# Kernel tuning notes

Hardware: AMD Instinct MI355X
Metric: run time of the kernel (lower is better)

## Reference

```python
import jax, jax.numpy as jnp
import numpy as np
import math

B, S, H, NH, WIN = 2, 2048, 1024, 16, 1024
HD = H // NH


def _ln(x, g, b, eps=1e-5):
    mu = jnp.mean(x, axis=-1, keepdims=True)
    var = jnp.var(x, axis=-1, keepdims=True)
    return (x - mu) * jax.lax.rsqrt(var + eps) * g + b


def setup_inputs() -> dict:
    key = jax.random.key(0)
    ks = jax.random.split(key, 16)
    w = lambda k, shp: jax.random.normal(k, shp, dtype=jnp.float32) * 0.02
    d = {
        "hidden_states": jax.random.normal(ks[0], (B, S, H), dtype=jnp.float32),
        "window_pos_bias": jax.random.normal(ks[1], (1, NH, 2 * WIN + 1, 2 * WIN + 1), dtype=jnp.float32) * 0.02,
        # position_encoding: Linear(1->H) + LayerNorm(H)
        "pe_w": w(ks[2], (1, H)), "pe_b": jnp.zeros((H,), jnp.float32),
        "pe_g": jnp.ones((H,), jnp.float32), "pe_beta": jnp.zeros((H,), jnp.float32),
        # pre-attention LayerNorm
        "norm_g": jnp.ones((H,), jnp.float32), "norm_b": jnp.zeros((H,), jnp.float32),
        # QKV projections (stored as [in, out])
        "Wq": w(ks[3], (H, H)), "bq": jnp.zeros((H,), jnp.float32),
        "Wk": w(ks[4], (H, H)), "bk": jnp.zeros((H,), jnp.float32),
        "Wv": w(ks[5], (H, H)), "bv": jnp.zeros((H,), jnp.float32),
        # out_proj: Linear(H,2H)+LN+ReLU, Linear(2H,2H)+LN+ReLU, Linear(2H,2H)+LN+ReLU, Linear(2H,H)
        "W1": w(ks[6], (H, 2 * H)), "b1": jnp.zeros((2 * H,), jnp.float32),
        "g1": jnp.ones((2 * H,), jnp.float32), "be1": jnp.zeros((2 * H,), jnp.float32),
        "W2": w(ks[7], (2 * H, 2 * H)), "b2": jnp.zeros((2 * H,), jnp.float32),
        "g2": jnp.ones((2 * H,), jnp.float32), "be2": jnp.zeros((2 * H,), jnp.float32),
        "W3": w(ks[8], (2 * H, 2 * H)), "b3": jnp.zeros((2 * H,), jnp.float32),
        "g3": jnp.ones((2 * H,), jnp.float32), "be3": jnp.zeros((2 * H,), jnp.float32),
        "W4": w(ks[9], (2 * H, H)), "b4": jnp.zeros((H,), jnp.float32),
    }
    return d


def reference(hidden_states, window_pos_bias, pe_w, pe_b, pe_g, pe_beta,
              norm_g, norm_b, Wq, bq, Wk, bk, Wv, bv,
              W1, b1, g1, be1, W2, b2, g2, be2, W3, b3, g3, be3, W4, b4):
    b, s, h = hidden_states.shape
    nh = window_pos_bias.shape[1]
    hd = h // nh
    # relative positions in [-1, 1): (i - s//2) / (s//2 + 1e-6)
    mid = s // 2
    pos = ((jnp.arange(s, dtype=jnp.float32) - mid) / (mid + 1e-6))[:, None]  # [s,1]
    pe = _ln(pos @ pe_w + pe_b, pe_g, pe_beta)  # [s,h]  (dropout = identity in eval)
    x = _ln(hidden_states + pe[None], norm_g, norm_b)
    q = (x @ Wq + bq).reshape(b, s, nh, hd)
    k = (x @ Wk + bk).reshape(b, s, nh, hd)
    v = (x @ Wv + bv).reshape(b, s, nh, hd)
    scores = jnp.einsum('bqhd,bkhd->bhqk', q, k) / math.sqrt(hd)
    if s <= window_pos_bias.shape[-1]:
        scores = scores + window_pos_bias[:, :, :s, :s]
    attn = jax.nn.softmax(scores, axis=-1)
    ctx = jnp.einsum('bhqk,bkhd->bqhd', attn, v).reshape(b, s, h)
    y = jax.nn.relu(_ln(ctx @ W1 + b1, g1, be1))
    y = jax.nn.relu(_ln(y @ W2 + b2, g2, be2))
    y = jax.nn.relu(_ln(y @ W3 + b3, g3, be3))
    out = y @ W4 + b4
    return out
```

## Files before the change

### kernel.cpp

```cpp
#include <hip/hip_runtime.h>
#include <hip/hip_bf16.h>
#include <math.h>

typedef unsigned short u16;
typedef unsigned int u32;
typedef __bf16 v8bf __attribute__((ext_vector_type(8)));
typedef float v4f __attribute__((ext_vector_type(4)));

constexpr int BATCH = 2;
constexpr int SEQ = 2048;
constexpr int HID = 1024;
constexpr int NHEAD = 16;
constexpr int HDIM = 64;
constexpr int MROWS = BATCH * SEQ;
constexpr int BIAS_LD = 2 * 1024 + 1;
constexpr size_t BIAS_HSTRIDE = (size_t)BIAS_LD * BIAS_LD;

__device__ __forceinline__ u16 f2bf(float f) {
    u32 u = __builtin_bit_cast(u32, f);
    u32 r = u + 0x7fffu + ((u >> 16) & 1u);
    return (u16)(r >> 16);
}

__device__ __forceinline__ int swoff8(int row, int chunk)  { return (row * 8  + (chunk ^ (row & 7)))  << 4; }
__device__ __forceinline__ int swoff16(int row, int chunk) { return (row * 16 + (chunk ^ (row & 15))) << 4; }

__device__ __forceinline__ float2 blockreduce2(float a, float b) {
    #pragma unroll
    for (int m = 1; m < 64; m <<= 1) {
        a += __shfl_xor(a, m, 64);
        b += __shfl_xor(b, m, 64);
    }
    __shared__ float la[4], lb[4];
    int w = threadIdx.x >> 6;
    if ((threadIdx.x & 63) == 0) { la[w] = a; lb[w] = b; }
    __syncthreads();
    a = la[0] + la[1] + la[2] + la[3];
    b = lb[0] + lb[1] + lb[2] + lb[3];
    __syncthreads();
    return make_float2(a, b);
}

__global__ __launch_bounds__(256) void k_wt(const float* __restrict__ W, u16* __restrict__ Wt, int K, int N) {
    __shared__ float t[32][33];
    int n0 = blockIdx.x * 32, k0 = blockIdx.y * 32;
    int tx = threadIdx.x & 31, ty = threadIdx.x >> 5;
    #pragma unroll
    for (int i = 0; i < 32; i += 8) t[ty + i][tx] = W[(size_t)(k0 + ty + i) * N + n0 + tx];
    __syncthreads();
    #pragma unroll
    for (int i = 0; i < 32; i += 8) Wt[(size_t)(n0 + ty + i) * K + k0 + tx] = f2bf(t[tx][ty + i]);
}

__global__ __launch_bounds__(256) void k_prenorm(const float* __restrict__ hidden,
        const float* __restrict__ pe_w, const float* __restrict__ pe_b,
        const float* __restrict__ pe_g, const float* __restrict__ pe_beta,
        const float* __restrict__ ng, const float* __restrict__ nb, u16* __restrict__ xbf) {
    int row = blockIdx.x;
    int s = row & (SEQ - 1);
    float pos = ((float)s - 1024.0f) * (1.0f / 1024.0f);
    int t = threadIdx.x;
    float v[4];
    float s1 = 0.f, s2 = 0.f;
    #pragma unroll
    for (int i = 0; i < 4; i++) {
        int hh = i * 256 + t;
        float x = pos * pe_w[hh] + pe_b[hh];
        v[i] = x; s1 += x; s2 += x * x;
    }
    float2 red = blockreduce2(s1, s2);
    float mean = red.x * (1.f / HID);
    float var  = red.y * (1.f / HID) - mean * mean;
    float rstd = rsqrtf(var + 1e-5f);
    s1 = 0.f; s2 = 0.f;
    #pragma unroll
    for (int i = 0; i < 4; i++) {
        int hh = i * 256 + t;
        float pe = (v[i] - mean) * rstd * pe_g[hh] + pe_beta[hh];
        float x = hidden[(size_t)row * HID + hh] + pe;
        v[i] = x; s1 += x; s2 += x * x;
    }
    red = blockreduce2(s1, s2);
    mean = red.x * (1.f / HID);
    var  = red.y * (1.f / HID) - mean * mean;
    rstd = rsqrtf(var + 1e-5f);
    #pragma unroll
    for (int i = 0; i < 4; i++) {
        int hh = i * 256 + t;
        xbf[(size_t)row * HID + hh] = f2bf((v[i] - mean) * rstd * ng[hh] + nb[hh]);
    }
}

__global__ __launch_bounds__(256) void k_ln_relu(const float* __restrict__ Z,
        const float* __restrict__ g, const float* __restrict__ be, u16* __restrict__ Y, int N) {
    int row = blockIdx.x, t = threadIdx.x;
    float v[8];
    float s1 = 0.f, s2 = 0.f;
    int c = N >> 8;
    #pragma unroll
    for (int i = 0; i < 8; i++) {
        if (i < c) {
            int hh = i * 256 + t;
            float x = Z[(size_t)row * N + hh];
            v[i] = x; s1 += x; s2 += x * x;
        }
    }
    float2 red = blockreduce2(s1, s2);
    float inv = 1.0f / (float)N;
    float mean = red.x * inv;
    float var  = red.y * inv - mean * mean;
    float rstd = rsqrtf(var + 1e-5f);
    #pragma unroll
    for (int i = 0; i < 8; i++) {
        if (i < c) {
            int hh = i * 256 + t;
            float y = (v[i] - mean) * rstd * g[hh] + be[hh];
            Y[(size_t)row * N + hh] = f2bf(fmaxf(y, 0.f));
        }
    }
}

__global__ __launch_bounds__(256) void k_vtrans(const u16* __restrict__ V, u16* __restrict__ Vt) {
    __shared__ u16 t[64][68];
    int s0 = blockIdx.x * 64, h = blockIdx.y, b = blockIdx.z;
    int x = threadIdx.x & 63, y = threadIdx.x >> 6;
    #pragma unroll
    for (int i = 0; i < 64; i += 4) {
        int r = i + y;
        t[r][x] = V[(size_t)(b * SEQ + s0 + r) * HID + h * HDIM + x];
    }
    __syncthreads();
    size_t ob = (size_t)(b * NHEAD + h) * HDIM;
    #pragma unroll
    for (int i = 0; i < 64; i += 4) {
        int d = i + y;
        Vt[(ob + d) * SEQ + s0 + x] = t[x][d];
    }
}

template <int OUT_BF16>
__global__ __launch_bounds__(256) void k_gemm(const u16* __restrict__ A, const u16* __restrict__ Bt,
        const float* __restrict__ bias, void* __restrict__ C, int N, int K, float scale) {
    __shared__ __align__(16) u16 lA[128 * 64];
    __shared__ __align__(16) u16 lB[128 * 64];
    char* lAc = (char*)lA;
    char* lBc = (char*)lB;
    const int m0 = blockIdx.x * 128, n0 = blockIdx.y * 128;
    const int tid = threadIdx.x, wave = tid >> 6, lane = tid & 63;
    const int wr = wave >> 1, wc = wave & 1, q4 = lane >> 4, ml = lane & 15;

    v4f acc[4][4];
    v4f zz = {0.f, 0.f, 0.f, 0.f};
    #pragma unroll
    for (int i = 0; i < 4; i++)
        #pragma unroll
        for (int j = 0; j < 4; j++) acc[i][j] = zz;

    for (int k0 = 0; k0 < K; k0 += 64) {
        __syncthreads();
        #pragma unroll
        for (int it = 0; it < 4; it++) {
            int c = tid + it * 256;
            int r = c >> 3, qc = c & 7;
            *(uint4*)(lAc + swoff8(r, qc)) = *(const uint4*)(A + (size_t)(m0 + r) * K + k0 + (qc << 3));
            *(uint4*)(lBc + swoff8(r, qc)) = *(const uint4*)(Bt + (size_t)(n0 + r) * K + k0 + (qc << 3));
        }
        __syncthreads();
        #pragma unroll
        for (int kk = 0; kk < 2; kk++) {
            v8bf af[4], bfv[4];
            #pragma unroll
            for (int i = 0; i < 4; i++) af[i] = *(const v8bf*)(lAc + swoff8(wr * 64 + i * 16 + ml, kk * 4 + q4));
            #pragma unroll
            for (int j = 0; j < 4; j++) bfv[j] = *(const v8bf*)(lBc + swoff8(wc * 64 + j * 16 + ml, kk * 4 + q4));
            #pragma unroll
            for (int i = 0; i < 4; i++)
                #pragma unroll
                for (int j = 0; j < 4; j++)
                    acc[i][j] = __builtin_amdgcn_mfma_f32_16x16x32_bf16(af[i], bfv[j], acc[i][j], 0, 0, 0);
        }
    }
    #pragma unroll
    for (int i = 0; i < 4; i++) {
        int rb = m0 + wr * 64 + i * 16 + q4 * 4;
        #pragma unroll
        for (int j = 0; j < 4; j++) {
            int col = n0 + wc * 64 + j * 16 + ml;
            float bv = bias[col];
            #pragma unroll
            for (int r = 0; r < 4; r++) {
                float val = (acc[i][j][r] + bv) * scale;
                if (OUT_BF16) ((u16*)C)[(size_t)(rb + r) * N + col] = f2bf(val);
                else          ((float*)C)[(size_t)(rb + r) * N + col] = val;
            }
        }
    }
}

__global__ __launch_bounds__(256) void k_attn(const u16* __restrict__ Qm, const u16* __restrict__ Km,
        const u16* __restrict__ Vtm, const float* __restrict__ bias, u16* __restrict__ ctx) {
    __shared__ __align__(16) u16 lK[128 * 64];
    __shared__ __align__(16) u16 lV[64 * 128];
    __shared__ __align__(16) u16 lP[4][32 * 128];
    int b = blockIdx.x, qt = blockIdx.y, h = blockIdx.z;
    int tid = threadIdx.x, wave = tid >> 6, lane = tid & 63;
    int q4 = lane >> 4, ml = lane & 15;
    char* lKc = (char*)lK;
    char* lVc = (char*)lV;
    char* lPc = (char*)lP[wave];

    v8bf qf[2][2];
    #pragma unroll
    for (int i = 0; i < 2; i++)
        #pragma unroll
        for (int kk = 0; kk < 2; kk++) {
            size_t row = (size_t)(b * SEQ + qt * 128 + wave * 32 + i * 16 + ml);
            qf[i][kk] = *(const v8bf*)(Qm + row * HID + h * HDIM + kk * 32 + q4 * 8);
        }

    float mr[2][4], lr[2][4];
    v4f o[2][4];
    v4f zz = {0.f, 0.f, 0.f, 0.f};
    #pragma unroll
    for (int i = 0; i < 2; i++)
        #pragma unroll
        for (int r = 0; r < 4; r++) { mr[i][r] = -1e30f; lr[i][r] = 0.f; }
    #pragma unroll
    for (int i = 0; i < 2; i++)
        #pragma unroll
        for (int n = 0; n < 4; n++) o[i][n] = zz;

    const float* bh = bias + (size_t)h * BIAS_HSTRIDE;
    const u16* Kb = Km + (size_t)b * SEQ * HID + h * HDIM;
    const u16* Vb = Vtm + (size_t)(b * NHEAD + h) * HDIM * SEQ;

    for (int kt = 0; kt < SEQ / 128; ++kt) {
        int k0 = kt * 128;
        __syncthreads();
        #pragma unroll
        for (int it = 0; it < 4; it++) {
            int c = tid + it * 256;
            {
                int r = c >> 3, qc = c & 7;
                *(uint4*)(lKc + swoff8(r, qc)) = *(const uint4*)(Kb + (size_t)(k0 + r) * HID + (qc << 3));
            }
            {
                int r = c >> 4, qc = c & 15;
                *(uint4*)(lVc + swoff16(r, qc)) = *(const uint4*)(Vb + (size_t)r * SEQ + k0 + (qc << 3));
            }
        }
        __syncthreads();

        v4f sa[2][8];
        #pragma unroll
        for (int i = 0; i < 2; i++)
            #pragma unroll
            for (int j = 0; j < 8; j++) sa[i][j] = zz;
        #pragma unroll
        for (int j = 0; j < 8; j++) {
            v8bf kf0 = *(const v8bf*)(lKc + swoff8(j * 16 + ml, q4));
            v8bf kf1 = *(const v8bf*)(lKc + swoff8(j * 16 + ml, 4 + q4));
            #pragma unroll
            for (int i = 0; i < 2; i++) {
                sa[i][j] = __builtin_amdgcn_mfma_f32_16x16x32_bf16(qf[i][0], kf0, sa[i][j], 0, 0, 0);
                sa[i][j] = __builtin_amdgcn_mfma_f32_16x16x32_bf16(qf[i][1], kf1, sa[i][j], 0, 0, 0);
            }
        }
        int qg0 = qt * 128 + wave * 32;
        #pragma unroll
        for (int i = 0; i < 2; i++)
            #pragma unroll
            for (int j = 0; j < 8; j++) {
                const float* bp = bh + (size_t)(qg0 + i * 16 + q4 * 4) * BIAS_LD + (k0 + j * 16 + ml);
                #pragma unroll
                for (int r = 0; r < 4; r++) sa[i][j][r] += bp[(size_t)r * BIAS_LD];
            }
        #pragma unroll
        for (int i = 0; i < 2; i++)
            #pragma unroll
            for (int r = 0; r < 4; r++) {
                float mx = sa[i][0][r];
                #pragma unroll
                for (int j = 1; j < 8; j++) mx = fmaxf(mx, sa[i][j][r]);
                mx = fmaxf(mx, __shfl_xor(mx, 1, 64));
                mx = fmaxf(mx, __shfl_xor(mx, 2, 64));
                mx = fmaxf(mx, __shfl_xor(mx, 4, 64));
                mx = fmaxf(mx, __shfl_xor(mx, 8, 64));
                float mnew = fmaxf(mr[i][r], mx);
                float alpha = __expf(mr[i][r] - mnew);
                mr[i][r] = mnew;
                float rs = 0.f;
                #pragma unroll
                for (int j = 0; j < 8; j++) {
                    float p = __expf(sa[i][j][r] - mnew);
                    sa[i][j][r] = p;
                    rs += p;
                }
                rs += __shfl_xor(rs, 1, 64);
                rs += __shfl_xor(rs, 2, 64);
                rs += __shfl_xor(rs, 4, 64);
                rs += __shfl_xor(rs, 8, 64);
                lr[i][r] = lr[i][r] * alpha + rs;
                #pragma unroll
                for (int n = 0; n < 4; n++) o[i][n][r] *= alpha;
            }
        #pragma unroll
        for (int i = 0; i < 2; i++)
            #pragma unroll
            for (int j = 0; j < 8; j++) {
                int col = j * 16 + ml;
                #pragma unroll
                for (int r = 0; r < 4; r++) {
                    int row = i * 16 + q4 * 4 + r;
                    int off = row * 256 + ((((col >> 3)) ^ (row & 15)) << 4) + ((col & 7) << 1);
                    *(u16*)(lPc + off) = f2bf(sa[i][j][r]);
                }
            }
        #pragma unroll
        for (int kk = 0; kk < 4; kk++) {
            v8bf pf[2];
            #pragma unroll
            for (int i = 0; i < 2; i++)
                pf[i] = *(const v8bf*)(lPc + swoff16(i * 16 + ml, kk * 4 + q4));
            #pragma unroll
            for (int n = 0; n < 4; n++) {
                v8bf vf = *(const v8bf*)(lVc + swoff16(n * 16 + ml, kk * 4 + q4));
                #pragma unroll
                for (int i = 0; i < 2; i++)
                    o[i][n] = __builtin_amdgcn_mfma_f32_16x16x32_bf16(pf[i], vf, o[i][n], 0, 0, 0);
            }
        }
    }
    #pragma unroll
    for (int i = 0; i < 2; i++)
        #pragma unroll
        for (int n = 0; n < 4; n++)
            #pragma unroll
            for (int r = 0; r < 4; r++) {
                float val = o[i][n][r] / lr[i][r];
                size_t row = (size_t)(b * SEQ + qt * 128 + wave * 32 + i * 16 + q4 * 4 + r);
                ctx[row * HID + h * HDIM + n * 16 + ml] = f2bf(val);
            }
}

extern "C" void kernel_launch(void* const* d_in, const int* in_sizes, int n_in,
                              void* d_out, int out_size, void* d_ws, size_t ws_size,
                              hipStream_t stream) {
    const float* hidden = (const float*)d_in[0];
    const float* wbias  = (const float*)d_in[1];
    const float* pe_w   = (const float*)d_in[2];
    const float* pe_b   = (const float*)d_in[3];
    const float* pe_g   = (const float*)d_in[4];
    const float* pe_be  = (const float*)d_in[5];
    const float* ng     = (const float*)d_in[6];
    const float* nb     = (const float*)d_in[7];
    const float* Wq = (const float*)d_in[8];  const float* bq = (const float*)d_in[9];
    const float* Wk = (const float*)d_in[10]; const float* bk = (const float*)d_in[11];
    const float* Wv = (const float*)d_in[12]; const float* bv = (const float*)d_in[13];
    const float* W1 = (const float*)d_in[14]; const float* b1 = (const float*)d_in[15];
    const float* g1 = (const float*)d_in[16]; const float* be1 = (const float*)d_in[17];
    const float* W2 = (const float*)d_in[18]; const float* b2 = (const float*)d_in[19];
    const float* g2 = (const float*)d_in[20]; const float* be2 = (const float*)d_in[21];
    const float* W3 = (const float*)d_in[22]; const float* b3 = (const float*)d_in[23];
    const float* g3 = (const float*)d_in[24]; const float* be3 = (const float*)d_in[25];
    const float* W4 = (const float*)d_in[26]; const float* b4 = (const float*)d_in[27];

    char* ws = (char*)d_ws;
    size_t off = 0;
    auto alloc = [&](size_t bytes) {
        char* p = ws + off;
        off += (bytes + 1023) & ~(size_t)1023;
        return p;
    };
    u16* wqt = (u16*)alloc((size_t)1024 * 1024 * 2);
    u16* wkt = (u16*)alloc((size_t)1024 * 1024 * 2);
    u16* wvt = (u16*)alloc((size_t)1024 * 1024 * 2);
    u16* w1t = (u16*)alloc((size_t)2048 * 1024 * 2);
    u16* w2t = (u16*)alloc((size_t)2048 * 2048 * 2);
    u16* w3t = (u16*)alloc((size_t)2048 * 2048 * 2);
    u16* w4t = (u16*)alloc((size_t)1024 * 2048 * 2);
    u16* xbf = (u16*)alloc((size_t)MROWS * HID * 2);
    char* qkv_region = ws + off;
    u16* qbf = (u16*)alloc((size_t)MROWS * HID * 2);
    u16* kbf = (u16*)alloc((size_t)MROWS * HID * 2);
    u16* vbf = (u16*)alloc((size_t)MROWS * HID * 2);
    u16* vtb = (u16*)alloc((size_t)MROWS * HID * 2);
    u16* ctx = (u16*)alloc((size_t)MROWS * HID * 2);
    u16* y1  = (u16*)alloc((size_t)MROWS * 2048 * 2);
    u16* y2  = (u16*)alloc((size_t)MROWS * 2048 * 2);
    float* z = (float*)qkv_region;

    dim3 blk(256);
    k_wt<<<dim3(32, 32), blk, 0, stream>>>(Wq, wqt, 1024, 1024);
    k_wt<<<dim3(32, 32), blk, 0, stream>>>(Wk, wkt, 1024, 1024);
    k_wt<<<dim3(32, 32), blk, 0, stream>>>(Wv, wvt, 1024, 1024);
    k_wt<<<dim3(64, 32), blk, 0, stream>>>(W1, w1t, 1024, 2048);
    k_wt<<<dim3(64, 64), blk, 0, stream>>>(W2, w2t, 2048, 2048);
    k_wt<<<dim3(64, 64), blk, 0, stream>>>(W3, w3t, 2048, 2048);
    k_wt<<<dim3(32, 64), blk, 0, stream>>>(W4, w4t, 2048, 1024);
    k_prenorm<<<MROWS, blk, 0, stream>>>(hidden, pe_w, pe_b, pe_g, pe_be, ng, nb, xbf);
    k_gemm<1><<<dim3(32, 8), blk, 0, stream>>>(xbf, wqt, bq, qbf, 1024, 1024, 0.125f);
    k_gemm<1><<<dim3(32, 8), blk, 0, stream>>>(xbf, wkt, bk, kbf, 1024, 1024, 1.0f);
    k_gemm<1><<<dim3(32, 8), blk, 0, stream>>>(xbf, wvt, bv, vbf, 1024, 1024, 1.0f);
    k_vtrans<<<dim3(32, 16, 2), blk, 0, stream>>>(vbf, vtb);
    k_attn<<<dim3(2, 16, 16), blk, 0, stream>>>(qbf, kbf, vtb, wbias, ctx);
    k_gemm<0><<<dim3(32, 16), blk, 0, stream>>>(ctx, w1t, b1, z, 2048, 1024, 1.0f);
    k_ln_relu<<<MROWS, blk, 0, stream>>>(z, g1, be1, y1, 2048);
    k_gemm<0><<<dim3(32, 16), blk, 0, stream>>>(y1, w2t, b2, z, 2048, 2048, 1.0f);
    k_ln_relu<<<MROWS, blk, 0, stream>>>(z, g2, be2, y2, 2048);
    k_gemm<0><<<dim3(32, 16), blk, 0, stream>>>(y2, w3t, b3, z, 2048, 2048, 1.0f);
    k_ln_relu<<<MROWS, blk, 0, stream>>>(z, g3, be3, y1, 2048);
    k_gemm<0><<<dim3(32, 8), blk, 0, stream>>>(y1, w4t, b4, (float*)d_out, 1024, 2048, 1.0f);
}
```

Baseline: 904.3 us.

## Fuse QKV GEMM, use direct-to-LDS loads, restructure attention, bf16 intermediates

New measurement: 897.9 us. Within noise of the previous version (-0.7%).

```diff
diff --git a/kernel.cpp b/kernel.cpp
--- a/kernel.cpp
+++ b/kernel.cpp
@@ -1,5 +1,6 @@
 #include <hip/hip_runtime.h>
 #include <hip/hip_bf16.h>
+#include <stdint.h>
 #include <math.h>
 
 typedef unsigned short u16;
@@ -13,6 +14,7 @@
 constexpr int NHEAD = 16;
 constexpr int HDIM = 64;
 constexpr int MROWS = BATCH * SEQ;
+constexpr int QKV_LD = 3 * HID;
 constexpr int BIAS_LD = 2 * 1024 + 1;
 constexpr size_t BIAS_HSTRIDE = (size_t)BIAS_LD * BIAS_LD;
 
@@ -20,6 +22,16 @@
     u32 u = __builtin_bit_cast(u32, f);
     u32 r = u + 0x7fffu + ((u >> 16) & 1u);
     return (u16)(r >> 16);
+}
+__device__ __forceinline__ float bf2f(u16 h) {
+    return __builtin_bit_cast(float, (u32)h << 16);
+}
+
+__device__ __forceinline__ void gld16(const void* g, void* lds_base) {
+    __builtin_amdgcn_global_load_lds(
+        (const __attribute__((address_space(1))) u32*)(uintptr_t)g,
+        (__attribute__((address_space(3))) u32*)(u32)(uintptr_t)lds_base,
+        16, 0, 0);
 }
 
 __device__ __forceinline__ int swoff8(int row, int chunk)  { return (row * 8  + (chunk ^ (row & 7)))  << 4; }
@@ -41,7 +53,8 @@
     return make_float2(a, b);
 }
 
-__global__ __launch_bounds__(256) void k_wt(const float* __restrict__ W, u16* __restrict__ Wt, int K, int N) {
+__global__ __launch_bounds__(256) void k_wt(const float* __restrict__ W, u16* __restrict__ Wt,
+                                            int K, int N, float scale) {
     __shared__ float t[32][33];
     int n0 = blockIdx.x * 32, k0 = blockIdx.y * 32;
     int tx = threadIdx.x & 31, ty = threadIdx.x >> 5;
@@ -49,7 +62,14 @@
     for (int i = 0; i < 32; i += 8) t[ty + i][tx] = W[(size_t)(k0 + ty + i) * N + n0 + tx];
     __syncthreads();
     #pragma unroll
-    for (int i = 0; i < 32; i += 8) Wt[(size_t)(n0 + ty + i) * K + k0 + tx] = f2bf(t[tx][ty + i]);
+    for (int i = 0; i < 32; i += 8) Wt[(size_t)(n0 + ty + i) * K + k0 + tx] = f2bf(t[tx][ty + i] * scale);
+}
+
+__global__ __launch_bounds__(256) void k_bcat(const float* __restrict__ bq, const float* __restrict__ bk,
+                                              const float* __restrict__ bv, float* __restrict__ o) {
+    int n = blockIdx.x * 256 + threadIdx.x;
+    float v = (n < 1024) ? bq[n] * 0.125f : (n < 2048 ? bk[n - 1024] : bv[n - 2048]);
+    o[n] = v;
 }
 
 __global__ __launch_bounds__(256) void k_prenorm(const float* __restrict__ hidden,
@@ -59,75 +79,73 @@
     int row = blockIdx.x;
     int s = row & (SEQ - 1);
     float pos = ((float)s - 1024.0f) * (1.0f / 1024.0f);
-    int t = threadIdx.x;
-    float v[4];
+    int t = threadIdx.x, hh = t * 4;
+    float4 pw = *(const float4*)(pe_w + hh);
+    float4 pb = *(const float4*)(pe_b + hh);
+    float v[4] = { pos * pw.x + pb.x, pos * pw.y + pb.y, pos * pw.z + pb.z, pos * pw.w + pb.w };
     float s1 = 0.f, s2 = 0.f;
     #pragma unroll
-    for (int i = 0; i < 4; i++) {
-        int hh = i * 256 + t;
-        float x = pos * pe_w[hh] + pe_b[hh];
-        v[i] = x; s1 += x; s2 += x * x;
-    }
+    for (int i = 0; i < 4; i++) { s1 += v[i]; s2 += v[i] * v[i]; }
     float2 red = blockreduce2(s1, s2);
     float mean = red.x * (1.f / HID);
     float var  = red.y * (1.f / HID) - mean * mean;
     float rstd = rsqrtf(var + 1e-5f);
+    float4 pg = *(const float4*)(pe_g + hh);
+    float4 pbe = *(const float4*)(pe_beta + hh);
+    float4 hv = *(const float4*)(hidden + (size_t)row * HID + hh);
+    v[0] = hv.x + (v[0] - mean) * rstd * pg.x + pbe.x;
+    v[1] = hv.y + (v[1] - mean) * rstd * pg.y + pbe.y;
+    v[2] = hv.z + (v[2] - mean) * rstd * pg.z + pbe.z;
+    v[3] = hv.w + (v[3] - mean) * rstd * pg.w + pbe.w;
     s1 = 0.f; s2 = 0.f;
     #pragma unroll
-    for (int i = 0; i < 4; i++) {
-        int hh = i * 256 + t;
-        float pe = (v[i] - mean) * rstd * pe_g[hh] + pe_beta[hh];
-        float x = hidden[(size_t)row * HID + hh] + pe;
-        v[i] = x; s1 += x; s2 += x * x;
-    }
+    for (int i = 0; i < 4; i++) { s1 += v[i]; s2 += v[i] * v[i]; }
     red = blockreduce2(s1, s2);
     mean = red.x * (1.f / HID);
     var  = red.y * (1.f / HID) - mean * mean;
     rstd = rsqrtf(var + 1e-5f);
-    #pragma unroll
-    for (int i = 0; i < 4; i++) {
-        int hh = i * 256 + t;
-        xbf[(size_t)row * HID + hh] = f2bf((v[i] - mean) * rstd * ng[hh] + nb[hh]);
-    }
-}
-
-__global__ __launch_bounds__(256) void k_ln_relu(const float* __restrict__ Z,
-        const float* __restrict__ g, const float* __restrict__ be, u16* __restrict__ Y, int N) {
-    int row = blockIdx.x, t = threadIdx.x;
+    float4 gg = *(const float4*)(ng + hh);
+    float4 bb = *(const float4*)(nb + hh);
+    ushort4 o;
+    o.x = f2bf((v[0] - mean) * rstd * gg.x + bb.x);
+    o.y = f2bf((v[1] - mean) * rstd * gg.y + bb.y);
+    o.z = f2bf((v[2] - mean) * rstd * gg.z + bb.z);
+    o.w = f2bf((v[3] - mean) * rstd * gg.w + bb.w);
+    *(ushort4*)(xbf + (size_t)row * HID + hh) = o;
+}
+
+__global__ __launch_bounds__(256) void k_ln_relu(const u16* __restrict__ Z,
+        const float* __restrict__ g, const float* __restrict__ be, u16* __restrict__ Y) {
+    const int N = 2048;
+    int row = blockIdx.x, t = threadIdx.x, base = t * 8;
+    union { uint4 q; u16 h[8]; } u;
+    u.q = *(const uint4*)(Z + (size_t)row * N + base);
     float v[8];
     float s1 = 0.f, s2 = 0.f;
-    int c = N >> 8;
-    #pragma unroll
-    for (int i = 0; i < 8; i++) {
-        if (i < c) {
-            int hh = i * 256 + t;
-            float x = Z[(size_t)row * N + hh];
-            v[i] = x; s1 += x; s2 += x * x;
-        }
-    }
+    #pragma unroll
+    for (int i = 0; i < 8; i++) { v[i] = bf2f(u.h[i]); s1 += v[i]; s2 += v[i] * v[i]; }
     float2 red = blockreduce2(s1, s2);
-    float inv = 1.0f / (float)N;
-    float mean = red.x * inv;
-    float var  = red.y * inv - mean * mean;
+    float mean = red.x * (1.f / N);
+    float var  = red.y * (1.f / N) - mean * mean;
     float rstd = rsqrtf(var + 1e-5f);
-    #pragma unroll
-    for (int i = 0; i < 8; i++) {
-        if (i < c) {
-            int hh = i * 256 + t;
-            float y = (v[i] - mean) * rstd * g[hh] + be[hh];
-            Y[(size_t)row * N + hh] = f2bf(fmaxf(y, 0.f));
-        }
-    }
-}
-
-__global__ __launch_bounds__(256) void k_vtrans(const u16* __restrict__ V, u16* __restrict__ Vt) {
+    float4 g0 = *(const float4*)(g + base), g1 = *(const float4*)(g + base + 4);
+    float4 b0 = *(const float4*)(be + base), b1 = *(const float4*)(be + base + 4);
+    float gg[8] = { g0.x, g0.y, g0.z, g0.w, g1.x, g1.y, g1.z, g1.w };
+    float bb[8] = { b0.x, b0.y, b0.z, b0.w, b1.x, b1.y, b1.z, b1.w };
+    union { uint4 q; u16 h[8]; } o;
+    #pragma unroll
+    for (int i = 0; i < 8; i++) o.h[i] = f2bf(fmaxf((v[i] - mean) * rstd * gg[i] + bb[i], 0.f));
+    *(uint4*)(Y + (size_t)row * N + base) = o.q;
+}
+
+__global__ __launch_bounds__(256) void k_vtrans(const u16* __restrict__ QKV, u16* __restrict__ Vt) {
     __shared__ u16 t[64][68];
     int s0 = blockIdx.x * 64, h = blockIdx.y, b = blockIdx.z;
     int x = threadIdx.x & 63, y = threadIdx.x >> 6;
     #pragma unroll
     for (int i = 0; i < 64; i += 4) {
         int r = i + y;
-        t[r][x] = V[(size_t)(b * SEQ + s0 + r) * HID + h * HDIM + x];
+        t[r][x] = QKV[(size_t)(b * SEQ + s0 + r) * QKV_LD + 2048 + h * HDIM + x];
     }
     __syncthreads();
     size_t ob = (size_t)(b * NHEAD + h) * HDIM;
@@ -139,8 +157,8 @@
 }
 
 template <int OUT_BF16>
-__global__ __launch_bounds__(256) void k_gemm(const u16* __restrict__ A, const u16* __restrict__ Bt,
-        const float* __restrict__ bias, void* __restrict__ C, int N, int K, float scale) {
+__global__ __launch_bounds__(256, 3) void k_gemm(const u16* __restrict__ A, const u16* __restrict__ Bt,
+        const float* __restrict__ bias, void* __restrict__ C, int N, int K) {
     __shared__ __align__(16) u16 lA[128 * 64];
     __shared__ __align__(16) u16 lB[128 * 64];
     char* lAc = (char*)lA;
@@ -148,6 +166,8 @@
     const int m0 = blockIdx.x * 128, n0 = blockIdx.y * 128;
     const int tid = threadIdx.x, wave = tid >> 6, lane = tid & 63;
     const int wr = wave >> 1, wc = wave & 1, q4 = lane >> 4, ml = lane & 15;
+    const int srow = wave * 8 + (lane >> 3);
+    const int sqc  = (lane & 7) ^ (lane >> 3);
 
     v4f acc[4][4];
     v4f zz = {0.f, 0.f, 0.f, 0.f};
@@ -160,10 +180,9 @@
         __syncthreads();
         #pragma unroll
         for (int it = 0; it < 4; it++) {
-            int c = tid + it * 256;
-            int r = c >> 3, qc = c & 7;
-            *(uint4*)(lAc + swoff8(r, qc)) = *(const uint4*)(A + (size_t)(m0 + r) * K + k0 + (qc << 3));
-            *(uint4*)(lBc + swoff8(r, qc)) = *(const uint4*)(Bt + (size_t)(n0 + r) * K + k0 + (qc << 3));
+            int r = it * 32 + srow;
+            gld16(A  + (size_t)(m0 + r) * K + k0 + sqc * 8, lAc + (it * 32 + wave * 8) * 128);
+            gld16(Bt + (size_t)(n0 + r) * K + k0 + sqc * 8, lBc + (it * 32 + wave * 8) * 128);
         }
         __syncthreads();
         #pragma unroll
@@ -189,7 +208,7 @@
             float bv = bias[col];
             #pragma unroll
             for (int r = 0; r < 4; r++) {
-                float val = (acc[i][j][r] + bv) * scale;
+                float val = acc[i][j][r] + bv;
                 if (OUT_BF16) ((u16*)C)[(size_t)(rb + r) * N + col] = f2bf(val);
                 else          ((float*)C)[(size_t)(rb + r) * N + col] = val;
             }
@@ -197,150 +216,126 @@
     }
 }
 
-__global__ __launch_bounds__(256) void k_attn(const u16* __restrict__ Qm, const u16* __restrict__ Km,
+__global__ __launch_bounds__(256, 3) void k_attn(const u16* __restrict__ QKV,
         const u16* __restrict__ Vtm, const float* __restrict__ bias, u16* __restrict__ ctx) {
     __shared__ __align__(16) u16 lK[128 * 64];
-    __shared__ __align__(16) u16 lV[64 * 128];
-    __shared__ __align__(16) u16 lP[4][32 * 128];
+    __shared__ __align__(16) u16 lP[4][16 * 128];
     int b = blockIdx.x, qt = blockIdx.y, h = blockIdx.z;
     int tid = threadIdx.x, wave = tid >> 6, lane = tid & 63;
     int q4 = lane >> 4, ml = lane & 15;
     char* lKc = (char*)lK;
-    char* lVc = (char*)lV;
     char* lPc = (char*)lP[wave];
-
-    v8bf qf[2][2];
-    #pragma unroll
-    for (int i = 0; i < 2; i++)
-        #pragma unroll
-        for (int kk = 0; kk < 2; kk++) {
-            size_t row = (size_t)(b * SEQ + qt * 128 + wave * 32 + i * 16 + ml);
-            qf[i][kk] = *(const v8bf*)(Qm + row * HID + h * HDIM + kk * 32 + q4 * 8);
-        }
-
-    float mr[2][4], lr[2][4];
-    v4f o[2][4];
+    const int qbase = qt * 64 + wave * 16;
+    const int srow = wave * 8 + (lane >> 3);
+    const int sqc  = (lane & 7) ^ (lane >> 3);
+
+    const u16* Qb = QKV + (size_t)(b * SEQ) * QKV_LD + h * HDIM;
+    const u16* Kb = QKV + (size_t)(b * SEQ) * QKV_LD + 1024 + h * HDIM;
+    const u16* Vb = Vtm + (size_t)(b * NHEAD + h) * HDIM * SEQ;
+    const float* bh = bias + (size_t)h * BIAS_HSTRIDE;
+
+    v8bf qf[2];
+    #pragma unroll
+    for (int kk = 0; kk < 2; kk++)
+        qf[kk] = *(const v8bf*)(Qb + (size_t)(qbase + ml) * QKV_LD + kk * 32 + q4 * 8);
+
+    float mr[4], lr[4];
+    v4f o[4];
     v4f zz = {0.f, 0.f, 0.f, 0.f};
     #pragma unroll
-    for (int i = 0; i < 2; i++)
-        #pragma unroll
-        for (int r = 0; r < 4; r++) { mr[i][r] = -1e30f; lr[i][r] = 0.f; }
-    #pragma unroll
-    for (int i = 0; i < 2; i++)
-        #pragma unroll
-        for (int n = 0; n < 4; n++) o[i][n] = zz;
-
-    const float* bh = bias + (size_t)h * BIAS_HSTRIDE;
-    const u16* Kb = Km + (size_t)b * SEQ * HID + h * HDIM;
-    const u16* Vb = Vtm + (size_t)(b * NHEAD + h) * HDIM * SEQ;
+    for (int r = 0; r < 4; r++) { mr[r] = -1e30f; lr[r] = 0.f; }
+    #pragma unroll
+    for (int n = 0; n < 4; n++) o[n] = zz;
 
     for (int kt = 0; kt < SEQ / 128; ++kt) {
         int k0 = kt * 128;
         __syncthreads();
         #pragma unroll
         for (int it = 0; it < 4; it++) {
-            int c = tid + it * 256;
-            {
-                int r = c >> 3, qc = c & 7;
-                *(uint4*)(lKc + swoff8(r, qc)) = *(const uint4*)(Kb + (size_t)(k0 + r) * HID + (qc << 3));
-            }
-            {
-                int r = c >> 4, qc = c & 15;
-                *(uint4*)(lVc + swoff16(r, qc)) = *(const uint4*)(Vb + (size_t)r * SEQ + k0 + (qc << 3));
-            }
-        }
+            int r = it * 32 + srow;
+            gld16(Kb + (size_t)(k0 + r) * QKV_LD + sqc * 8, lKc + (it * 32 + wave * 8) * 128);
+        }
+        float bv[4][8];
+        const float* bp0 = bh + (size_t)(qbase + q4 * 4) * BIAS_LD + k0 + ml;
+        #pragma unroll
+        for (int r = 0; r < 4; r++)
+            #pragma unroll
+            for (int j = 0; j < 8; j++) bv[r][j] = bp0[(size_t)r * BIAS_LD + j * 16];
         __syncthreads();
 
-        v4f sa[2][8];
-        #pragma unroll
-        for (int i = 0; i < 2; i++)
-            #pragma unroll
-            for (int j = 0; j < 8; j++) sa[i][j] = zz;
+        v4f sa[8];
+        #pragma unroll
+        for (int j = 0; j < 8; j++) sa[j] = zz;
         #pragma unroll
         for (int j = 0; j < 8; j++) {
             v8bf kf0 = *(const v8bf*)(lKc + swoff8(j * 16 + ml, q4));
             v8bf kf1 = *(const v8bf*)(lKc + swoff8(j * 16 + ml, 4 + q4));
-            #pragma unroll
-            for (int i = 0; i < 2; i++) {
-                sa[i][j] = __builtin_amdgcn_mfma_f32_16x16x32_bf16(qf[i][0], kf0, sa[i][j], 0, 0, 0);
-                sa[i][j] = __builtin_amdgcn_mfma_f32_16x16x32_bf16(qf[i][1], kf1, sa[i][j], 0, 0, 0);
+            sa[j] = __builtin_amdgcn_mfma_f32_16x16x32_bf16(qf[0], kf0, sa[j], 0, 0, 0);
+            sa[j] = __builtin_amdgcn_mfma_f32_16x16x32_bf16(qf[1], kf1, sa[j], 0, 0, 0);
+        }
+        #pragma unroll
+        for (int r = 0; r < 4; r++) {
+            float mx = -1e30f;
+            #pragma unroll
+            for (int j = 0; j < 8; j++) { sa[j][r] += bv[r][j]; mx = fmaxf(mx, sa[j][r]); }
+            mx = fmaxf(mx, __shfl_xor(mx, 1, 64));
+            mx = fmaxf(mx, __shfl_xor(mx, 2, 64));
+            mx = fmaxf(mx, __shfl_xor(mx, 4, 64));
+            mx = fmaxf(mx, __shfl_xor(mx, 8, 64));
+            float mnew = fmaxf(mr[r], mx);
+            float alpha = __expf(mr[r] - mnew);
+            mr[r] = mnew;
+            float rs = 0.f;
+            #pragma unroll
+            for (int j = 0; j < 8; j++) {
+                float p = __expf(sa[j][r] - mnew);
+                sa[j][r] = p;
+                rs += p;
             }
-        }
-        int qg0 = qt * 128 + wave * 32;
-        #pragma unroll
-        for (int i = 0; i < 2; i++)
-            #pragma unroll
-            for (int j = 0; j < 8; j++) {
-                const float* bp = bh + (size_t)(qg0 + i * 16 + q4 * 4) * BIAS_LD + (k0 + j * 16 + ml);
+            rs += __shfl_xor(rs, 1, 64);
+            rs += __shfl_xor(rs, 2, 64);
+            rs += __shfl_xor(rs, 4, 64);
+            rs += __shfl_xor(rs, 8, 64);
+            lr[r] = lr[r] * alpha + rs;
+            #pragma unroll
+            for (int n = 0; n < 4; n++) o[n][r] *= alpha;
+        }
+        #pragma unroll
+        for (int j = 0; j < 8; j++) {
+            int col = j * 16 + ml;
+            #pragma unroll
+            for (int r = 0; r < 4; r++) {
+                int row = q4 * 4 + r;
+                int off = row * 256 + (((col >> 3) ^ row) << 4) + ((col & 7) << 1);
+                *(u16*)(lPc + off) = f2bf(sa[j][r]);
+            }
+        }
+        v8bf vfc[4], vfn[4];
+        #pragma unroll
+        for (int n = 0; n < 4; n++)
+            vfc[n] = *(const v8bf*)(Vb + (size_t)(n * 16 + ml) * SEQ + k0 + q4 * 8);
+        #pragma unroll
+        for (int kk = 0; kk < 4; kk++) {
+            if (kk < 3) {
                 #pragma unroll
-                for (int r = 0; r < 4; r++) sa[i][j][r] += bp[(size_t)r * BIAS_LD];
+                for (int n = 0; n < 4; n++)
+                    vfn[n] = *(const v8bf*)(Vb + (size_t)(n * 16 + ml) * SEQ + k0 + (kk + 1) * 32 + q4 * 8);
             }
-        #pragma unroll
-        for (int i = 0; i < 2; i++)
-            #pragma unroll
-            for (int r = 0; r < 4; r++) {
-                float mx = sa[i][0][r];
-                #pragma unroll
-                for (int j = 1; j < 8; j++) mx = fmaxf(mx, sa[i][j][r]);
-                mx = fmaxf(mx, __shfl_xor(mx, 1, 64));
-                mx = fmaxf(mx, __shfl_xor(mx, 2, 64));
-                mx = fmaxf(mx, __shfl_xor(mx, 4, 64));
-                mx = fmaxf(mx, __shfl_xor(mx, 8, 64));
-                float mnew = fmaxf(mr[i][r], mx);
-                float alpha = __expf(mr[i][r] - mnew);
-                mr[i][r] = mnew;
-                float rs = 0.f;
-                #pragma unroll
-                for (int j = 0; j < 8; j++) {
-                    float p = __expf(sa[i][j][r] - mnew);
-                    sa[i][j][r] = p;
-                    rs += p;
-                }
-                rs += __shfl_xor(rs, 1, 64);
-                rs += __shfl_xor(rs, 2, 64);
-                rs += __shfl_xor(rs, 4, 64);
-                rs += __shfl_xor(rs, 8, 64);
-                lr[i][r] = lr[i][r] * alpha + rs;
-                #pragma unroll
-                for (int n = 0; n < 4; n++) o[i][n][r] *= alpha;
-            }
-        #pragma unroll
-        for (int i = 0; i < 2; i++)
-            #pragma unroll
-            for (int j = 0; j < 8; j++) {
-                int col = j * 16 + ml;
-                #pragma unroll
-                for (int r = 0; r < 4; r++) {
-                    int row = i * 16 + q4 * 4 + r;
-                    int off = row * 256 + ((((col >> 3)) ^ (row & 15)) << 4) + ((col & 7) << 1);
-                    *(u16*)(lPc + off) = f2bf(sa[i][j][r]);
-                }
-            }
-        #pragma unroll
-        for (int kk = 0; kk < 4; kk++) {
-            v8bf pf[2];
-            #pragma unroll
-            for (int i = 0; i < 2; i++)
-                pf[i] = *(const v8bf*)(lPc + swoff16(i * 16 + ml, kk * 4 + q4));
-            #pragma unroll
-            for (int n = 0; n < 4; n++) {
-                v8bf vf = *(const v8bf*)(lVc + swoff16(n * 16 + ml, kk * 4 + q4));
-                #pragma unroll
-                for (int i = 0; i < 2; i++)
-                    o[i][n] = __builtin_amdgcn_mfma_f32_16x16x32_bf16(pf[i], vf, o[i][n], 0, 0, 0);
-            }
-        }
-    }
-    #pragma unroll
-    for (int i = 0; i < 2; i++)
-        #pragma unroll
-        for (int n = 0; n < 4; n++)
-            #pragma unroll
-            for (int r = 0; r < 4; r++) {
-                float val = o[i][n][r] / lr[i][r];
-                size_t row = (size_t)(b * SEQ + qt * 128 + wave * 32 + i * 16 + q4 * 4 + r);
-                ctx[row * HID + h * HDIM + n * 16 + ml] = f2bf(val);
-            }
+            v8bf pf = *(const v8bf*)(lPc + swoff16(ml, kk * 4 + q4));
+            #pragma unroll
+            for (int n = 0; n < 4; n++)
+                o[n] = __builtin_amdgcn_mfma_f32_16x16x32_bf16(pf, vfc[n], o[n], 0, 0, 0);
+            #pragma unroll
+            for (int n = 0; n < 4; n++) vfc[n] = vfn[n];
+        }
+    }
+    #pragma unroll
+    for (int n = 0; n < 4; n++)
+        #pragma unroll
+        for (int r = 0; r < 4; r++) {
+            size_t row = (size_t)(b * SEQ + qbase + q4 * 4 + r);
+            ctx[row * HID + h * HDIM + n * 16 + ml] = f2bf(o[n][r] / lr[r]);
+        }
 }
 
 extern "C" void kernel_launch(void* const* d_in, const int* in_sizes, int n_in,
@@ -372,43 +367,38 @@
         off += (bytes + 1023) & ~(size_t)1023;
         return p;
     };
-    u16* wqt = (u16*)alloc((size_t)1024 * 1024 * 2);
-    u16* wkt = (u16*)alloc((size_t)1024 * 1024 * 2);
-    u16* wvt = (u16*)alloc((size_t)1024 * 1024 * 2);
+    u16* wqkvt = (u16*)alloc((size_t)3072 * 1024 * 2);
     u16* w1t = (u16*)alloc((size_t)2048 * 1024 * 2);
     u16* w2t = (u16*)alloc((size_t)2048 * 2048 * 2);
     u16* w3t = (u16*)alloc((size_t)2048 * 2048 * 2);
     u16* w4t = (u16*)alloc((size_t)1024 * 2048 * 2);
+    float* bqkv = (float*)alloc((size_t)3072 * 4);
     u16* xbf = (u16*)alloc((size_t)MROWS * HID * 2);
-    char* qkv_region = ws + off;
-    u16* qbf = (u16*)alloc((size_t)MROWS * HID * 2);
-    u16* kbf = (u16*)alloc((size_t)MROWS * HID * 2);
-    u16* vbf = (u16*)alloc((size_t)MROWS * HID * 2);
+    u16* qkv = (u16*)alloc((size_t)MROWS * QKV_LD * 2);
     u16* vtb = (u16*)alloc((size_t)MROWS * HID * 2);
     u16* ctx = (u16*)alloc((size_t)MROWS * HID * 2);
-    u16* y1  = (u16*)alloc((size_t)MROWS * 2048 * 2);
-    u16* y2  = (u16*)alloc((size_t)MROWS * 2048 * 2);
-    float* z = (float*)qkv_region;
+    u16* zb  = (u16*)alloc((size_t)MROWS * 2048 * 2);
+    u16* ya  = (u16*)alloc((size_t)MROWS * 2048 * 2);
+    u16* yb  = (u16*)alloc((size_t)MROWS * 2048 * 2);
 
     dim3 blk(256);
-    k_wt<<<dim3(32, 32), blk, 0, stream>>>(Wq, wqt, 1024, 1024);
-    k_wt<<<dim3(32, 32), blk, 0, stream>>>(Wk, wkt, 1024, 1024);
-    k_wt<<<dim3(32, 32), blk, 0, stream>>>(Wv, wvt, 1024, 1024);
-    k_wt<<<dim3(64, 32), blk, 0, stream>>>(W1, w1t, 1024, 2048);
-    k_wt<<<dim3(64, 64), blk, 0, stream>>>(W2, w2t, 2048, 2048);
-    k_wt<<<dim3(64, 64), blk, 0, stream>>>(W3, w3t, 2048, 2048);
-    k_wt<<<dim3(32, 64), blk, 0, stream>>>(W4, w4t, 2048, 1024);
+    k_wt<<<dim3(32, 32), blk, 0, stream>>>(Wq, wqkvt, 1024, 1024, 0.125f);
+    k_wt<<<dim3(32, 32), blk, 0, stream>>>(Wk, wqkvt + (size_t)1024 * 1024, 1024, 1024, 1.0f);
+    k_wt<<<dim3(32, 32), blk, 0, stream>>>(Wv, wqkvt + (size_t)2048 * 1024, 1024, 1024, 1.0f);
+    k_wt<<<dim3(64, 32), blk, 0, stream>>>(W1, w1t, 1024, 2048, 1.0f);
+    k_wt<<<dim3(64, 64), blk, 0, stream>>>(W2, w2t, 2048, 2048, 1.0f);
+    k_wt<<<dim3(64, 64), blk, 0, stream>>>(W3, w3t, 2048, 2048, 1.0f);
+    k_wt<<<dim3(32, 64), blk, 0, stream>>>(W4, w4t, 2048, 1024, 1.0f);
+    k_bcat<<<dim3(12), blk, 0, stream>>>(bq, bk, bv, bqkv);
     k_prenorm<<<MROWS, blk, 0, stream>>>(hidden, pe_w, pe_b, pe_g, pe_be, ng, nb, xbf);
-    k_gemm<1><<<dim3(32, 8), blk, 0, stream>>>(xbf, wqt, bq, qbf, 1024, 1024, 0.125f);
-    k_gemm<1><<<dim3(32, 8), blk, 0, stream>>>(xbf, wkt, bk, kbf, 1024, 1024, 1.0f);
-    k_gemm<1><<<dim3(32, 8), blk, 0, stream>>>(xbf, wvt, bv, vbf, 1024, 1024, 1.0f);
-    k_vtrans<<<dim3(32, 16, 2), blk, 0, stream>>>(vbf, vtb);
-    k_attn<<<dim3(2, 16, 16), blk, 0, stream>>>(qbf, kbf, vtb, wbias, ctx);
-    k_gemm<0><<<dim3(32, 16), blk, 0, stream>>>(ctx, w1t, b1, z, 2048, 1024, 1.0f);
-    k_ln_relu<<<MROWS, blk, 0, stream>>>(z, g1, be1, y1, 2048);
-    k_gemm<0><<<dim3(32, 16), blk, 0, stream>>>(y1, w2t, b2, z, 2048, 2048, 1.0f);
-    k_ln_relu<<<MROWS, blk, 0, stream>>>(z, g2, be2, y2, 2048);
-    k_gemm<0><<<dim3(32, 16), blk, 0, stream>>>(y2, w3t, b3, z, 2048, 2048, 1.0f);
-    k_ln_relu<<<MROWS, blk, 0, stream>>>(z, g3, be3, y1, 2048);
-    k_gemm<0><<<dim3(32, 8), blk, 0, stream>>>(y1, w4t, b4, (float*)d_out, 1024, 2048, 1.0f);
-}
+    k_gemm<1><<<dim3(32, 24), blk, 0, stream>>>(xbf, wqkvt, bqkv, qkv, QKV_LD, 1024);
+    k_vtrans<<<dim3(32, 16, 2), blk, 0, stream>>>(qkv, vtb);
+    k_attn<<<dim3(2, 32, 16), blk, 0, stream>>>(qkv, vtb, wbias, ctx);
+    k_gemm<1><<<dim3(32, 16), blk, 0, stream>>>(ctx, w1t, b1, zb, 2048, 1024);
+    k_ln_relu<<<MROWS, blk, 0, stream>>>(zb, g1, be1, ya);
+    k_gemm<1><<<dim3(32, 16), blk, 0, stream>>>(ya, w2t, b2, zb, 2048, 2048);
+    k_ln_relu<<<MROWS, blk, 0, stream>>>(zb, g2, be2, yb);
+    k_gemm<1><<<dim3(32, 16), blk, 0, stream>>>(yb, w3t, b3, zb, 2048, 2048);
+    k_ln_relu<<<MROWS, blk, 0, stream>>>(zb, g3, be3, ya);
+    k_gemm<0><<<dim3(32, 8), blk, 0, stream>>>(ya, w4t, b4, (float*)d_out, 1024, 2048);
+}
```
